# Kernel tuning notes

Measured on AMD Instinct MI355X. Metric: run time of the kernel, lower is better.

The kernel has to match this reference:

```python
import jax, jax.numpy as jnp
import numpy as np

B, N, C, H = 2, 2048, 1024, 16
D = C // H
SCALE = D ** -0.5


def setup_inputs() -> dict:
    key = jax.random.key(0)
    ks = jax.random.split(key, 4)
    s = 0.02
    return {
        "x": jax.random.normal(ks[0], (B, N, C), dtype=jnp.float32),
        "f": jax.random.normal(ks[1], (B, N, C), dtype=jnp.float32),
        "W_qkv": jax.random.normal(ks[2], (C, 3 * C), dtype=jnp.float32) * s,
        "W_proj": jax.random.normal(ks[3], (C, C), dtype=jnp.float32) * s,
        "b_proj": jnp.zeros((C,), dtype=jnp.float32),
    }


def reference(x, f, W_qkv, W_proj, b_proj):
    b, n, c = x.shape
    h, d = H, c // H
    # qkv projection -> (B,N,3,H,D) -> q,k,v each (B,H,N,D)
    qkv = (x @ W_qkv).reshape(b, n, 3, h, d)
    q = jnp.transpose(qkv[:, :, 0], (0, 2, 1, 3))
    k = jnp.transpose(qkv[:, :, 1], (0, 2, 1, 3))
    v = jnp.transpose(qkv[:, :, 2], (0, 2, 1, 3))
    # full NxN scores, faithful to the original manual MHA
    attn = jax.nn.softmax(jnp.einsum("bhqd,bhkd->bhqk", q, k) * SCALE, axis=-1)
    av = jnp.einsum("bhqk,bhkd->bhqd", attn, v)  # (B,H,N,D)
    # pre-residual output branch
    attn2gcn = jnp.transpose(av, (0, 2, 1, 3)).reshape(b, n, c)
    # residual fuse with f (reshaped per-head in torch; equivalent to flat add)
    fused = attn2gcn + f
    out = fused @ W_proj + b_proj
    return (out, attn2gcn)
```

## Files before the change

### kernel.cpp

```cpp
#include <hip/hip_runtime.h>
#include <hip/hip_bf16.h>

#define OUT1_OFF 4194304
#define QSCALE 0.1803368801111204f

typedef __attribute__((ext_vector_type(8))) short bf16x8;
typedef __attribute__((ext_vector_type(4))) float f32x4;

__device__ __forceinline__ unsigned short f2bf(float x) {
    unsigned u = __float_as_uint(x);
    u += 0x7FFFu + ((u >> 16) & 1u);
    return (unsigned short)(u >> 16);
}

__device__ __forceinline__ void gl2lds16(const unsigned short* g, unsigned short* l) {
    __builtin_amdgcn_global_load_lds(
        (const __attribute__((address_space(1))) unsigned int*)g,
        (__attribute__((address_space(3))) unsigned int*)l, 16, 0, 0);
}

__global__ __launch_bounds__(256) void prep(const float* __restrict__ x,
                                            const float* __restrict__ Wqkv,
                                            const float* __restrict__ Wproj,
                                            unsigned short* __restrict__ xb,
                                            unsigned short* __restrict__ wqkvT,
                                            unsigned short* __restrict__ wprojT) {
    __shared__ float T[64][65];
    const int bid = blockIdx.x, tid = threadIdx.x;
    if (bid < 4096) {
        int i = bid * 256 + tid;
        float4 v = reinterpret_cast<const float4*>(x)[i];
        ushort4 o = make_ushort4(f2bf(v.x), f2bf(v.y), f2bf(v.z), f2bf(v.w));
        reinterpret_cast<ushort4*>(xb)[i] = o;
        return;
    }
    const float* in; unsigned short* out; int Nd, bx, by;
    if (bid < 4864) { int t = bid - 4096; in = Wqkv;  out = wqkvT;  Nd = 3072; bx = t % 48; by = t / 48; }
    else            { int t = bid - 4864; in = Wproj; out = wprojT; Nd = 1024; bx = t % 16; by = t / 16; }
    const int Kd = 1024;
    const int r0 = by * 64, c0 = bx * 64;
    const int tr = tid >> 3, tc = (tid & 7) * 8;
#pragma unroll
    for (int rr = 0; rr < 64; rr += 32) {
        const float4* p = reinterpret_cast<const float4*>(&in[(r0 + tr + rr) * Nd + c0 + tc]);
        float4 v0 = p[0], v1 = p[1];
        T[tr + rr][tc + 0] = v0.x; T[tr + rr][tc + 1] = v0.y;
        T[tr + rr][tc + 2] = v0.z; T[tr + rr][tc + 3] = v0.w;
        T[tr + rr][tc + 4] = v1.x; T[tr + rr][tc + 5] = v1.y;
        T[tr + rr][tc + 6] = v1.z; T[tr + rr][tc + 7] = v1.w;
    }
    __syncthreads();
#pragma unroll
    for (int rr = 0; rr < 64; rr += 32) {
        int orow = tr + rr;
        ushort4 o0 = make_ushort4(f2bf(T[tc + 0][orow]), f2bf(T[tc + 1][orow]),
                                  f2bf(T[tc + 2][orow]), f2bf(T[tc + 3][orow]));
        ushort4 o1 = make_ushort4(f2bf(T[tc + 4][orow]), f2bf(T[tc + 5][orow]),
                                  f2bf(T[tc + 6][orow]), f2bf(T[tc + 7][orow]));
        unsigned short* dst = &out[(c0 + orow) * Kd + r0 + tc];
        *reinterpret_cast<ushort4*>(dst) = o0;
        *reinterpret_cast<ushort4*>(dst + 4) = o1;
    }
}

__global__ __launch_bounds__(256) void gemm_qkv(const unsigned short* __restrict__ A,
                                                const unsigned short* __restrict__ Bt,
                                                unsigned short* __restrict__ qb,
                                                unsigned short* __restrict__ kb,
                                                unsigned short* __restrict__ vtb) {
    __shared__ __align__(16) unsigned short Sh[32768];
    const int tid = threadIdx.x;
    const int w = tid >> 6, lane = tid & 63, quad = lane >> 4, l15 = lane & 15;
    const int m0 = blockIdx.y * 128, n0 = blockIdx.x * 128;
    const int wm = (w & 1) * 64, wn = (w >> 1) * 64;
    const int nbase = n0 + wn;
    const int t = nbase >> 10;
    const bool qk = (t < 2);
    const int sw = (l15 & 7) << 3;
    f32x4 acc[4][4] = {};

#define QKV_STAGE(K0, BUF) do {                                               \
        unsigned short* As_ = &Sh[(BUF) * 16384];                             \
        unsigned short* Bs_ = As_ + 8192;                                     \
        _Pragma("unroll")                                                     \
        for (int tt = 0; tt < 4; ++tt) {                                      \
            int c = tt * 256 + tid;                                           \
            int row = c >> 3, jg = ((c & 7) ^ (row & 7)) * 8;                 \
            gl2lds16(&A[(m0 + row) * 1024 + (K0) + jg], &As_[c * 8]);         \
            gl2lds16(&Bt[(n0 + row) * 1024 + (K0) + jg], &Bs_[c * 8]);        \
        } } while (0)

    auto compute = [&](int buf) {
        const unsigned short* As_ = &Sh[buf * 16384];
        const unsigned short* Bs_ = As_ + 8192;
#pragma unroll
        for (int kk = 0; kk < 2; ++kk) {
            bf16x8 af[4], bfr[4];
#pragma unroll
            for (int i = 0; i < 4; ++i)
                af[i] = *reinterpret_cast<const bf16x8*>(
                    &As_[(wm + i * 16 + l15) * 64 + ((((kk * 4 + quad) << 3) ^ sw))]);
#pragma unroll
            for (int j = 0; j < 4; ++j)
                bfr[j] = *reinterpret_cast<const bf16x8*>(
                    &Bs_[(wn + j * 16 + l15) * 64 + ((((kk * 4 + quad) << 3) ^ sw))]);
            if (qk) {
#pragma unroll
                for (int i = 0; i < 4; ++i)
#pragma unroll
                    for (int j = 0; j < 4; ++j)
                        acc[i][j] = __builtin_amdgcn_mfma_f32_16x16x32_bf16(bfr[j], af[i], acc[i][j], 0, 0, 0);
            } else {
#pragma unroll
                for (int i = 0; i < 4; ++i)
#pragma unroll
                    for (int j = 0; j < 4; ++j)
                        acc[i][j] = __builtin_amdgcn_mfma_f32_16x16x32_bf16(af[i], bfr[j], acc[i][j], 0, 0, 0);
            }
        }
    };

    QKV_STAGE(0, 0);
    for (int k0 = 0; k0 < 1024; k0 += 128) {
        __syncthreads();
        QKV_STAGE(k0 + 64, 1);
        compute(0);
        __syncthreads();
        if (k0 + 128 < 1024) QKV_STAGE(k0 + 128, 0);
        compute(1);
    }
#undef QKV_STAGE
    __syncthreads();
    unsigned short* scr = Sh + w * 4608;
    const int mb = m0 + wm;
    const int b = mb >> 11;
    const int h = (nbase & 1023) >> 6;
    const float sc = (t == 0) ? QSCALE : 1.f;
    if (qk) {
#pragma unroll
        for (int i = 0; i < 4; ++i) {
            int row = i * 16 + l15;
#pragma unroll
            for (int j = 0; j < 4; ++j) {
                unsigned short h0 = f2bf(acc[i][j][0] * sc), h1 = f2bf(acc[i][j][1] * sc);
                unsigned short h2 = f2bf(acc[i][j][2] * sc), h3 = f2bf(acc[i][j][3] * sc);
                uint2 pk = make_uint2((unsigned)h0 | ((unsigned)h1 << 16),
                                      (unsigned)h2 | ((unsigned)h3 << 16));
                *reinterpret_cast<uint2*>(&scr[row * 72 + j * 16 + quad * 4]) = pk;
            }
        }
        asm volatile("s_waitcnt lgkmcnt(0)" ::: "memory");
        unsigned short* dst = (t == 0 ? qb : kb) + (((b * 16 + h) * 2048) + (mb & 2047)) * 64;
#pragma unroll
        for (int p = 0; p < 8; ++p) {
            int idx = p * 64 + lane;
            *reinterpret_cast<uint4*>(&dst[idx * 8]) =
                *reinterpret_cast<const uint4*>(&scr[(idx >> 3) * 72 + (idx & 7) * 8]);
        }
    } else {
        const int kblk = (mb & 2047) >> 6;
#pragma unroll
        for (int i = 0; i < 4; ++i) {
            int slot0 = ((i & 2) << 4) | (quad << 3) | ((i & 1) << 2);
#pragma unroll
            for (int j = 0; j < 4; ++j) {
                unsigned short h0 = f2bf(acc[i][j][0]), h1 = f2bf(acc[i][j][1]);
                unsigned short h2 = f2bf(acc[i][j][2]), h3 = f2bf(acc[i][j][3]);
                uint2 pk = make_uint2((unsigned)h0 | ((unsigned)h1 << 16),
                                      (unsigned)h2 | ((unsigned)h3 << 16));
                *reinterpret_cast<uint2*>(&scr[(j * 16 + l15) * 72 + slot0]) = pk;
            }
        }
        asm volatile("s_waitcnt lgkmcnt(0)" ::: "memory");
        unsigned short* vtile = vtb + (((b * 16 + h) * 32) + kblk) * 4096;
#pragma unroll
        for (int p = 0; p < 8; ++p) {
            int idx = p * 64 + lane;
            *reinterpret_cast<uint4*>(&vtile[idx * 8]) =
                *reinterpret_cast<const uint4*>(&scr[(idx >> 3) * 72 + (idx & 7) * 8]);
        }
    }
}

__global__ __launch_bounds__(512, 4) void attn_kernel(const unsigned short* __restrict__ qb,
                                                      const unsigned short* __restrict__ kb,
                                                      const unsigned short* __restrict__ vtb,
                                                      const float* __restrict__ f,
                                                      float* __restrict__ attn2_out,
                                                      unsigned short* __restrict__ fusedb) {
    __shared__ __align__(16) unsigned char SMEM[69632];
    unsigned short* S16 = reinterpret_cast<unsigned short*>(SMEM);
    const int tid = threadIdx.x;
    const int w = tid >> 6, lane = tid & 63, quad = lane >> 4, l15 = lane & 15;
    const int qg = w & 3, kh = w >> 2;
    const int bh = blockIdx.x;
    const int q0w = blockIdx.y * 128 + qg * 32;
    const unsigned short* qr = &qb[(bh * 2048 + q0w + l15) * 64 + quad * 8];
    bf16x8 ql0 = *reinterpret_cast<const bf16x8*>(qr);
    bf16x8 ql1 = *reinterpret_cast<const bf16x8*>(qr + 32);
    bf16x8 ql2 = *reinterpret_cast<const bf16x8*>(qr + 1024);
    bf16x8 ql3 = *reinterpret_cast<const bf16x8*>(qr + 1056);
    const unsigned short* kt0 = kb + bh * 131072;
    const unsigned short* vt0 = vtb + bh * 131072;
    const int gu = (((tid & ~7) | ((tid & 7) ^ ((tid >> 3) & 7))) << 3);
    const int sw = (l15 & 7) << 3;
    f32x4 O0[4] = {}, O1[4] = {};
    f32x4 asum0 = {}, asum1 = {};
    bf16x8 ones;
#pragma unroll
    for (int j = 0; j < 8; ++j) ones[j] = (short)0x3F80;

#define STAGE(IT, BUF) do { unsigned short* db_ = &S16[(BUF) * 16384 + tid * 8]; \
        const int go_ = (IT) * 4096 + gu;                                        \
        gl2lds16(kt0 + go_, db_);                                                \
        gl2lds16(vt0 + go_, db_ + 4096);                                         \
        gl2lds16(kt0 + 65536 + go_, db_ + 8192);                                 \
        gl2lds16(vt0 + 65536 + go_, db_ + 12288); } while (0)

    auto body = [&](int buf) {
        const unsigned short* Kb = &S16[buf * 16384 + kh * 8192];
        const unsigned short* Vb = Kb + 4096;
        f32x4 Ta[4], Tb[4];
        __builtin_amdgcn_s_setprio(1);
#pragma unroll
        for (int s = 0; s < 4; ++s) {
            const unsigned short* kr = &Kb[(s * 16 + l15) * 64];
            bf16x8 k0 = *reinterpret_cast<const bf16x8*>(&kr[(quad << 3) ^ sw]);
            bf16x8 k1 = *reinterpret_cast<const bf16x8*>(&kr[((quad + 4) << 3) ^ sw]);
            f32x4 za = {}, zb = {};
            za = __builtin_amdgcn_mfma_f32_16x16x32_bf16(k0, ql0, za, 0, 0, 0);
            za = __builtin_amdgcn_mfma_f32_16x16x32_bf16(k1, ql1, za, 0, 0, 0);
            zb = __builtin_amdgcn_mfma_f32_16x16x32_bf16(k0, ql2, zb, 0, 0, 0);
            zb = __builtin_amdgcn_mfma_f32_16x16x32_bf16(k1, ql3, zb, 0, 0, 0);
            Ta[s] = za; Tb[s] = zb;
        }
        __builtin_amdgcn_s_setprio(0);
        float pa_[4][4], pb_[4][4];
#pragma unroll
        for (int s = 0; s < 4; ++s)
#pragma unroll
            for (int r = 0; r < 4; ++r) {
                pa_[s][r] = __builtin_amdgcn_exp2f(Ta[s][r]);
                pb_[s][r] = __builtin_amdgcn_exp2f(Tb[s][r]);
            }
        uint4 u0, u1, v0u, v1u;
        u0.x = __builtin_amdgcn_perm(__float_as_uint(pa_[0][1]), __float_as_uint(pa_[0][0]), 0x07060302u);
        u0.y = __builtin_amdgcn_perm(__float_as_uint(pa_[0][3]), __float_as_uint(pa_[0][2]), 0x07060302u);
        u0.z = __builtin_amdgcn_perm(__float_as_uint(pa_[1][1]), __float_as_uint(pa_[1][0]), 0x07060302u);
        u0.w = __builtin_amdgcn_perm(__float_as_uint(pa_[1][3]), __float_as_uint(pa_[1][2]), 0x07060302u);
        u1.x = __builtin_amdgcn_perm(__float_as_uint(pa_[2][1]), __float_as_uint(pa_[2][0]), 0x07060302u);
        u1.y = __builtin_amdgcn_perm(__float_as_uint(pa_[2][3]), __float_as_uint(pa_[2][2]), 0x07060302u);
        u1.z = __builtin_amdgcn_perm(__float_as_uint(pa_[3][1]), __float_as_uint(pa_[3][0]), 0x07060302u);
        u1.w = __builtin_amdgcn_perm(__float_as_uint(pa_[3][3]), __float_as_uint(pa_[3][2]), 0x07060302u);
        v0u.x = __builtin_amdgcn_perm(__float_as_uint(pb_[0][1]), __float_as_uint(pb_[0][0]), 0x07060302u);
        v0u.y = __builtin_amdgcn_perm(__float_as_uint(pb_[0][3]), __float_as_uint(pb_[0][2]), 0x07060302u);
        v0u.z = __builtin_amdgcn_perm(__float_as_uint(pb_[1][1]), __float_as_uint(pb_[1][0]), 0x07060302u);
        v0u.w = __builtin_amdgcn_perm(__float_as_uint(pb_[1][3]), __float_as_uint(pb_[1][2]), 0x07060302u);
        v1u.x = __builtin_amdgcn_perm(__float_as_uint(pb_[2][1]), __float_as_uint(pb_[2][0]), 0x07060302u);
        v1u.y = __builtin_amdgcn_perm(__float_as_uint(pb_[2][3]), __float_as_uint(pb_[2][2]), 0x07060302u);
        v1u.z = __builtin_amdgcn_perm(__float_as_uint(pb_[3][1]), __float_as_uint(pb_[3][0]), 0x07060302u);
        v1u.w = __builtin_amdgcn_perm(__float_as_uint(pb_[3][3]), __float_as_uint(pb_[3][2]), 0x07060302u);
        bf16x8 paa0 = __builtin_bit_cast(bf16x8, u0);
        bf16x8 paa1 = __builtin_bit_cast(bf16x8, u1);
        bf16x8 pba0 = __builtin_bit_cast(bf16x8, v0u);
        bf16x8 pba1 = __builtin_bit_cast(bf16x8, v1u);
        asum0 = __builtin_amdgcn_mfma_f32_16x16x32_bf16(paa0, ones, asum0, 0, 0, 0);
        asum0 = __builtin_amdgcn_mfma_f32_16x16x32_bf16(paa1, ones, asum0, 0, 0, 0);
        asum1 = __builtin_amdgcn_mfma_f32_16x16x32_bf16(pba0, ones, asum1, 0, 0, 0);
        asum1 = __builtin_amdgcn_mfma_f32_16x16x32_bf16(pba1, ones, asum1, 0, 0, 0);
        __builtin_amdgcn_s_setprio(1);
#pragma unroll
        for (int c4 = 0; c4 < 4; ++c4) {
            const unsigned short* vr = &Vb[(c4 * 16 + l15) * 64];
            bf16x8 v0 = *reinterpret_cast<const bf16x8*>(&vr[(quad << 3) ^ sw]);
            bf16x8 v1 = *reinterpret_cast<const bf16x8*>(&vr[((quad + 4) << 3) ^ sw]);
            O0[c4] = __builtin_amdgcn_mfma_f32_16x16x32_bf16(paa0, v0, O0[c4], 0, 0, 0);
            O0[c4] = __builtin_amdgcn_mfma_f32_16x16x32_bf16(paa1, v1, O0[c4], 0, 0, 0);
            O1[c4] = __builtin_amdgcn_mfma_f32_16x16x32_bf16(pba0, v0, O1[c4], 0, 0, 0);
            O1[c4] = __builtin_amdgcn_mfma_f32_16x16x32_bf16(pba1, v1, O1[c4], 0, 0, 0);
        }
        __builtin_amdgcn_s_setprio(0);
    };

    STAGE(0, 0);
    for (int it = 0; it < 16; it += 2) {
        __syncthreads();
        STAGE(it + 1, 1);
        body(0);
        __syncthreads();
        if (it + 2 < 16) STAGE(it + 2, 0);
        body(1);
    }
#undef STAGE

    __syncthreads();
    float* scr = reinterpret_cast<float*>(SMEM);
    {
        float* myr = scr + w * 2176;
#pragma unroll
        for (int c4 = 0; c4 < 4; ++c4) {
            int dcol = c4 * 16 + l15;
#pragma unroll
            for (int r = 0; r < 4; ++r) {
                myr[(quad * 4 + r) * 68 + dcol] = O0[c4][r];
                myr[(16 + quad * 4 + r) * 68 + dcol] = O1[c4][r];
            }
        }
        if (l15 == 0) {
#pragma unroll
            for (int r = 0; r < 4; ++r) {
                myr[(quad * 4 + r) * 68 + 64] = asum0[r];
                myr[(16 + quad * 4 + r) * 68 + 64] = asum1[r];
            }
        }
    }
    __syncthreads();
    const int b = bh >> 4, h = bh & 15;
    const float* rA = scr + qg * 2176;
    const float* rB = rA + 4 * 2176;
    const int row = kh * 16 + (lane >> 2);
    const int dq = (lane & 3) * 16;
    const int base = (b * 2048 + (q0w + row)) * 1024 + h * 64;
    const float den = rA[row * 68 + 64] + rB[row * 68 + 64];
    const float inv = 1.f / den;
#pragma unroll
    for (int j = 0; j < 4; ++j) {
        int d = dq + j * 4;
        f32x4 pa = *reinterpret_cast<const f32x4*>(&rA[row * 68 + d]);
        f32x4 pb = *reinterpret_cast<const f32x4*>(&rB[row * 68 + d]);
        float4 fv = *reinterpret_cast<const float4*>(&f[base + d]);
        float o0 = (pa[0] + pb[0]) * inv;
        float o1 = (pa[1] + pb[1]) * inv;
        float o2 = (pa[2] + pb[2]) * inv;
        float o3 = (pa[3] + pb[3]) * inv;
        *reinterpret_cast<float4*>(&attn2_out[base + d]) = make_float4(o0, o1, o2, o3);
        ushort4 pk = make_ushort4(f2bf(o0 + fv.x), f2bf(o1 + fv.y),
                                  f2bf(o2 + fv.z), f2bf(o3 + fv.w));
        *reinterpret_cast<ushort4*>(&fusedb[base + d]) = pk;
    }
}

__global__ __launch_bounds__(256) void gemm_proj(const unsigned short* __restrict__ A,
                                                 const unsigned short* __restrict__ Bt,
                                                 const float* __restrict__ bias,
                                                 float* __restrict__ out) {
    __shared__ __align__(16) unsigned short Sh[24576];
    const int tid = threadIdx.x;
    const int w = tid >> 6, lane = tid & 63, quad = lane >> 4, l15 = lane & 15;
    const int m0 = blockIdx.y * 128, n0 = blockIdx.x * 64;
    const int wm = (w & 1) * 64, wn = (w >> 1) * 32;
    const int sw = (l15 & 7) << 3;
    f32x4 acc[4][2] = {};

#define PROJ_STAGE(K0, BUF) do {                                              \
        unsigned short* As_ = &Sh[(BUF) * 12288];                             \
        unsigned short* Bs_ = As_ + 8192;                                     \
        _Pragma("unroll")                                                     \
        for (int tt = 0; tt < 4; ++tt) {                                      \
            int c = tt * 256 + tid;                                           \
            int row = c >> 3, jg = ((c & 7) ^ (row & 7)) * 8;                 \
            gl2lds16(&A[(m0 + row) * 1024 + (K0) + jg], &As_[c * 8]);         \
            if (tt < 2) gl2lds16(&Bt[(n0 + row) * 1024 + (K0) + jg], &Bs_[c * 8]); \
        } } while (0)

    auto compute = [&](int buf) {
        const unsigned short* As_ = &Sh[buf * 12288];
        const unsigned short* Bs_ = As_ + 8192;
#pragma unroll
        for (int kk = 0; kk < 2; ++kk) {
            bf16x8 af[4], bfr[2];
#pragma unroll
            for (int i = 0; i < 4; ++i)
                af[i] = *reinterpret_cast<const bf16x8*>(
                    &As_[(wm + i * 16 + l15) * 64 + ((((kk * 4 + quad) << 3) ^ sw))]);
#pragma unroll
            for (int j = 0; j < 2; ++j)
                bfr[j] = *reinterpret_cast<const bf16x8*>(
                    &Bs_[(wn + j * 16 + l15) * 64 + ((((kk * 4 + quad) << 3) ^ sw))]);
#pragma unroll
            for (int i = 0; i < 4; ++i)
#pragma unroll
                for (int j = 0; j < 2; ++j)
                    acc[i][j] = __builtin_amdgcn_mfma_f32_16x16x32_bf16(af[i], bfr[j], acc[i][j], 0, 0, 0);
        }
    };

    PROJ_STAGE(0, 0);
    for (int k0 = 0; k0 < 1024; k0 += 128) {
        __syncthreads();
        PROJ_STAGE(k0 + 64, 1);
        compute(0);
        __syncthreads();
        if (k0 + 128 < 1024) PROJ_STAGE(k0 + 128, 0);
        compute(1);
    }
#undef PROJ_STAGE

#pragma unroll
    for (int j = 0; j < 2; ++j) {
        int n = n0 + wn + j * 16 + l15;
        float bv = bias[n];
#pragma unroll
        for (int i = 0; i < 4; ++i)
#pragma unroll
            for (int r = 0; r < 4; ++r) {
                int m = m0 + wm + i * 16 + quad * 4 + r;
                out[m * 1024 + n] = acc[i][j][r] + bv;
            }
    }
}

extern "C" void kernel_launch(void* const* d_in, const int* in_sizes, int n_in,
                              void* d_out, int out_size, void* d_ws, size_t ws_size,
                              hipStream_t stream) {
    const float* x      = (const float*)d_in[0];
    const float* f      = (const float*)d_in[1];
    const float* W_qkv  = (const float*)d_in[2];
    const float* W_proj = (const float*)d_in[3];
    const float* b_proj = (const float*)d_in[4];
    float* out   = (float*)d_out;
    float* attn2 = out + OUT1_OFF;

    char* ws = (char*)d_ws;
    unsigned short* xb     = (unsigned short*)(ws);
    unsigned short* wqkvT  = (unsigned short*)(ws + 8388608);
    unsigned short* wprojT = (unsigned short*)(ws + 14680064);
    unsigned short* qb     = (unsigned short*)(ws + 16777216);
    unsigned short* kb     = (unsigned short*)(ws + 25165824);
    unsigned short* vtb    = (unsigned short*)(ws + 33554432);
    unsigned short* fusedb = (unsigned short*)(ws + 41943040);

    prep<<<5120, 256, 0, stream>>>(x, W_qkv, W_proj, xb, wqkvT, wprojT);
    gemm_qkv<<<dim3(24, 32), 256, 0, stream>>>(xb, wqkvT, qb, kb, vtb);
    attn_kernel<<<dim3(32, 16), 512, 0, stream>>>(qb, kb, vtb, f, attn2, fusedb);
    gemm_proj<<<dim3(16, 32), 256, 0, stream>>>(fusedb, wprojT, b_proj, out);
}
```

Measured before the change: 176.2 us.

## Software-pipeline attention loop: overlap QK^T of tile i with PV of tile i-1

```diff
diff --git a/kernel.cpp b/kernel.cpp
--- a/kernel.cpp
+++ b/kernel.cpp
@@ -209,17 +209,43 @@
     bf16x8 ones;
 #pragma unroll
     for (int j = 0; j < 8; ++j) ones[j] = (short)0x3F80;
-
-#define STAGE(IT, BUF) do { unsigned short* db_ = &S16[(BUF) * 16384 + tid * 8]; \
+    bf16x8 pA0 = {}, pA1 = {}, pA2 = {}, pA3 = {};
+    bf16x8 pB0 = {}, pB1 = {}, pB2 = {}, pB3 = {};
+
+#define BARX() do { __builtin_amdgcn_sched_barrier(0); __builtin_amdgcn_s_barrier(); \
+                    __builtin_amdgcn_sched_barrier(0); } while (0)
+#define VMW(N) asm volatile("s_waitcnt vmcnt(" #N ")" ::: "memory")
+#define STAGE_K(IT, B) do { unsigned short* kd_ = &S16[(B) * 8192 + tid * 8];    \
         const int go_ = (IT) * 4096 + gu;                                        \
-        gl2lds16(kt0 + go_, db_);                                                \
-        gl2lds16(vt0 + go_, db_ + 4096);                                         \
-        gl2lds16(kt0 + 65536 + go_, db_ + 8192);                                 \
-        gl2lds16(vt0 + 65536 + go_, db_ + 12288); } while (0)
-
-    auto body = [&](int buf) {
-        const unsigned short* Kb = &S16[buf * 16384 + kh * 8192];
-        const unsigned short* Vb = Kb + 4096;
+        gl2lds16(kt0 + go_, kd_);                                                \
+        gl2lds16(kt0 + 65536 + go_, kd_ + 4096); } while (0)
+#define STAGE_V(IT, B) do { unsigned short* vd_ = &S16[16384 + (B) * 8192 + tid * 8]; \
+        const int go_ = (IT) * 4096 + gu;                                        \
+        gl2lds16(vt0 + go_, vd_);                                                \
+        gl2lds16(vt0 + 65536 + go_, vd_ + 4096); } while (0)
+
+    auto pv = [&](int vbb, bf16x8& i0, bf16x8& i1, bf16x8& i2, bf16x8& i3) {
+        const unsigned short* Vb = &S16[16384 + vbb * 8192 + kh * 4096];
+        asum0 = __builtin_amdgcn_mfma_f32_16x16x32_bf16(i0, ones, asum0, 0, 0, 0);
+        asum0 = __builtin_amdgcn_mfma_f32_16x16x32_bf16(i1, ones, asum0, 0, 0, 0);
+        asum1 = __builtin_amdgcn_mfma_f32_16x16x32_bf16(i2, ones, asum1, 0, 0, 0);
+        asum1 = __builtin_amdgcn_mfma_f32_16x16x32_bf16(i3, ones, asum1, 0, 0, 0);
+#pragma unroll
+        for (int c4 = 0; c4 < 4; ++c4) {
+            const unsigned short* vr = &Vb[(c4 * 16 + l15) * 64];
+            bf16x8 v0 = *reinterpret_cast<const bf16x8*>(&vr[(quad << 3) ^ sw]);
+            bf16x8 v1 = *reinterpret_cast<const bf16x8*>(&vr[((quad + 4) << 3) ^ sw]);
+            O0[c4] = __builtin_amdgcn_mfma_f32_16x16x32_bf16(i0, v0, O0[c4], 0, 0, 0);
+            O0[c4] = __builtin_amdgcn_mfma_f32_16x16x32_bf16(i1, v1, O0[c4], 0, 0, 0);
+            O1[c4] = __builtin_amdgcn_mfma_f32_16x16x32_bf16(i2, v0, O1[c4], 0, 0, 0);
+            O1[c4] = __builtin_amdgcn_mfma_f32_16x16x32_bf16(i3, v1, O1[c4], 0, 0, 0);
+        }
+    };
+
+    auto step = [&](int kbb, int vbb,
+                    bf16x8& i0, bf16x8& i1, bf16x8& i2, bf16x8& i3,
+                    bf16x8& o0, bf16x8& o1, bf16x8& o2, bf16x8& o3, bool doPV) {
+        const unsigned short* Kb = &S16[kbb * 8192 + kh * 4096];
         f32x4 Ta[4], Tb[4];
         __builtin_amdgcn_s_setprio(1);
 #pragma unroll
@@ -234,6 +260,7 @@
             zb = __builtin_amdgcn_mfma_f32_16x16x32_bf16(k1, ql3, zb, 0, 0, 0);
             Ta[s] = za; Tb[s] = zb;
         }
+        if (doPV) pv(vbb, i0, i1, i2, i3);
         __builtin_amdgcn_s_setprio(0);
         float pa_[4][4], pb_[4][4];
 #pragma unroll
@@ -260,38 +287,35 @@
         v1u.y = __builtin_amdgcn_perm(__float_as_uint(pb_[2][3]), __float_as_uint(pb_[2][2]), 0x07060302u);
         v1u.z = __builtin_amdgcn_perm(__float_as_uint(pb_[3][1]), __float_as_uint(pb_[3][0]), 0x07060302u);
         v1u.w = __builtin_amdgcn_perm(__float_as_uint(pb_[3][3]), __float_as_uint(pb_[3][2]), 0x07060302u);
-        bf16x8 paa0 = __builtin_bit_cast(bf16x8, u0);
-        bf16x8 paa1 = __builtin_bit_cast(bf16x8, u1);
-        bf16x8 pba0 = __builtin_bit_cast(bf16x8, v0u);
-        bf16x8 pba1 = __builtin_bit_cast(bf16x8, v1u);
-        asum0 = __builtin_amdgcn_mfma_f32_16x16x32_bf16(paa0, ones, asum0, 0, 0, 0);
-        asum0 = __builtin_amdgcn_mfma_f32_16x16x32_bf16(paa1, ones, asum0, 0, 0, 0);
-        asum1 = __builtin_amdgcn_mfma_f32_16x16x32_bf16(pba0, ones, asum1, 0, 0, 0);
-        asum1 = __builtin_amdgcn_mfma_f32_16x16x32_bf16(pba1, ones, asum1, 0, 0, 0);
-        __builtin_amdgcn_s_setprio(1);
-#pragma unroll
-        for (int c4 = 0; c4 < 4; ++c4) {
-            const unsigned short* vr = &Vb[(c4 * 16 + l15) * 64];
-            bf16x8 v0 = *reinterpret_cast<const bf16x8*>(&vr[(quad << 3) ^ sw]);
-            bf16x8 v1 = *reinterpret_cast<const bf16x8*>(&vr[((quad + 4) << 3) ^ sw]);
-            O0[c4] = __builtin_amdgcn_mfma_f32_16x16x32_bf16(paa0, v0, O0[c4], 0, 0, 0);
-            O0[c4] = __builtin_amdgcn_mfma_f32_16x16x32_bf16(paa1, v1, O0[c4], 0, 0, 0);
-            O1[c4] = __builtin_amdgcn_mfma_f32_16x16x32_bf16(pba0, v0, O1[c4], 0, 0, 0);
-            O1[c4] = __builtin_amdgcn_mfma_f32_16x16x32_bf16(pba1, v1, O1[c4], 0, 0, 0);
-        }
-        __builtin_amdgcn_s_setprio(0);
+        o0 = __builtin_bit_cast(bf16x8, u0);
+        o1 = __builtin_bit_cast(bf16x8, u1);
+        o2 = __builtin_bit_cast(bf16x8, v0u);
+        o3 = __builtin_bit_cast(bf16x8, v1u);
     };
 
-    STAGE(0, 0);
-    for (int it = 0; it < 16; it += 2) {
-        __syncthreads();
-        STAGE(it + 1, 1);
-        body(0);
-        __syncthreads();
-        if (it + 2 < 16) STAGE(it + 2, 0);
-        body(1);
-    }
-#undef STAGE
+    STAGE_K(0, 0); STAGE_V(0, 0); STAGE_K(1, 1);
+    VMW(2); BARX();
+    step(0, 0, pA0, pA1, pA2, pA3, pA0, pA1, pA2, pA3, false);
+    BARX(); STAGE_K(2, 0); STAGE_V(1, 1); VMW(4); BARX();
+    for (int i = 1; i < 13; i += 2) {
+        step(1, 0, pA0, pA1, pA2, pA3, pB0, pB1, pB2, pB3, true);
+        BARX(); STAGE_K(i + 2, 1); STAGE_V(i + 1, 0); VMW(4); BARX();
+        step(0, 1, pB0, pB1, pB2, pB3, pA0, pA1, pA2, pA3, true);
+        BARX(); STAGE_K(i + 3, 0); STAGE_V(i + 2, 1); VMW(4); BARX();
+    }
+    step(1, 0, pA0, pA1, pA2, pA3, pB0, pB1, pB2, pB3, true);
+    BARX(); STAGE_K(15, 1); STAGE_V(14, 0); VMW(4); BARX();
+    step(0, 1, pB0, pB1, pB2, pB3, pA0, pA1, pA2, pA3, true);
+    BARX(); STAGE_V(15, 1); VMW(2); BARX();
+    step(1, 0, pA0, pA1, pA2, pA3, pB0, pB1, pB2, pB3, true);
+    VMW(0); BARX();
+    __builtin_amdgcn_s_setprio(1);
+    pv(1, pB0, pB1, pB2, pB3);
+    __builtin_amdgcn_s_setprio(0);
+#undef STAGE_K
+#undef STAGE_V
+#undef BARX
+#undef VMW
 
     __syncthreads();
     float* scr = reinterpret_cast<float*>(SMEM);
```

Result: slower. 198.1 us (+12.4%).

## Restage QKV GEMM A-tile through registers to cut LDS and raise occupancy

Applied to the files above, without the earlier changes.

```diff
diff --git a/kernel.cpp b/kernel.cpp
--- a/kernel.cpp
+++ b/kernel.cpp
@@ -27,16 +27,20 @@
                                             unsigned short* __restrict__ wprojT) {
     __shared__ float T[64][65];
     const int bid = blockIdx.x, tid = threadIdx.x;
-    if (bid < 4096) {
-        int i = bid * 256 + tid;
-        float4 v = reinterpret_cast<const float4*>(x)[i];
-        ushort4 o = make_ushort4(f2bf(v.x), f2bf(v.y), f2bf(v.z), f2bf(v.w));
-        reinterpret_cast<ushort4*>(xb)[i] = o;
+    if (bid < 1024) {
+        int base = bid * 1024 + tid;
+#pragma unroll
+        for (int j = 0; j < 4; ++j) {
+            int i = base + j * 256;
+            float4 v = reinterpret_cast<const float4*>(x)[i];
+            ushort4 o = make_ushort4(f2bf(v.x), f2bf(v.y), f2bf(v.z), f2bf(v.w));
+            reinterpret_cast<ushort4*>(xb)[i] = o;
+        }
         return;
     }
     const float* in; unsigned short* out; int Nd, bx, by;
-    if (bid < 4864) { int t = bid - 4096; in = Wqkv;  out = wqkvT;  Nd = 3072; bx = t % 48; by = t / 48; }
-    else            { int t = bid - 4864; in = Wproj; out = wprojT; Nd = 1024; bx = t % 16; by = t / 16; }
+    if (bid < 1792) { int t = bid - 1024; in = Wqkv;  out = wqkvT;  Nd = 3072; bx = t % 48; by = t / 48; }
+    else            { int t = bid - 1792; in = Wproj; out = wprojT; Nd = 1024; bx = t % 16; by = t / 16; }
     const int Kd = 1024;
     const int r0 = by * 64, c0 = bx * 64;
     const int tr = tid >> 3, tc = (tid & 7) * 8;
@@ -63,12 +67,12 @@
     }
 }
 
-__global__ __launch_bounds__(256) void gemm_qkv(const unsigned short* __restrict__ A,
-                                                const unsigned short* __restrict__ Bt,
-                                                unsigned short* __restrict__ qb,
-                                                unsigned short* __restrict__ kb,
-                                                unsigned short* __restrict__ vtb) {
-    __shared__ __align__(16) unsigned short Sh[32768];
+__global__ __launch_bounds__(256, 3) void gemm_qkv(const unsigned short* __restrict__ A,
+                                                   const unsigned short* __restrict__ Bt,
+                                                   unsigned short* __restrict__ qb,
+                                                   unsigned short* __restrict__ kb,
+                                                   unsigned short* __restrict__ vtb) {
+    __shared__ __align__(16) unsigned short Sh[24576];
     const int tid = threadIdx.x;
     const int w = tid >> 6, lane = tid & 63, quad = lane >> 4, l15 = lane & 15;
     const int m0 = blockIdx.y * 128, n0 = blockIdx.x * 128;
@@ -78,21 +82,31 @@
     const bool qk = (t < 2);
     const int sw = (l15 & 7) << 3;
     f32x4 acc[4][4] = {};
-
-#define QKV_STAGE(K0, BUF) do {                                               \
-        unsigned short* As_ = &Sh[(BUF) * 16384];                             \
-        unsigned short* Bs_ = As_ + 8192;                                     \
-        _Pragma("unroll")                                                     \
-        for (int tt = 0; tt < 4; ++tt) {                                      \
-            int c = tt * 256 + tid;                                           \
-            int row = c >> 3, jg = ((c & 7) ^ (row & 7)) * 8;                 \
-            gl2lds16(&A[(m0 + row) * 1024 + (K0) + jg], &As_[c * 8]);         \
-            gl2lds16(&Bt[(n0 + row) * 1024 + (K0) + jg], &Bs_[c * 8]);        \
-        } } while (0)
+    int aoff[4], boff[4], loff[4];
+#pragma unroll
+    for (int tt = 0; tt < 4; ++tt) {
+        int c = tt * 256 + tid;
+        int row = c >> 3, jg = ((c & 7) ^ (row & 7)) * 8;
+        aoff[tt] = (m0 + row) * 1024 + jg;
+        boff[tt] = (n0 + row) * 1024 + jg;
+        loff[tt] = c * 8;
+    }
+    uint4 areg[4];
+
+#define VMW(N) asm volatile("s_waitcnt vmcnt(" #N ")" ::: "memory")
+#define LGK0() asm volatile("s_waitcnt lgkmcnt(0)" ::: "memory")
+#define BARX() do { __builtin_amdgcn_sched_barrier(0); __builtin_amdgcn_s_barrier(); \
+                    __builtin_amdgcn_sched_barrier(0); } while (0)
+#define LOAD_A(K0) do { _Pragma("unroll") for (int tt = 0; tt < 4; ++tt)          \
+        areg[tt] = *reinterpret_cast<const uint4*>(&A[aoff[tt] + (K0)]); } while (0)
+#define WRITE_A() do { _Pragma("unroll") for (int tt = 0; tt < 4; ++tt)           \
+        *reinterpret_cast<uint4*>(&Sh[loff[tt]]) = areg[tt]; } while (0)
+#define STAGE_B(K0, BUF) do { _Pragma("unroll") for (int tt = 0; tt < 4; ++tt)    \
+        gl2lds16(&Bt[boff[tt] + (K0)], &Sh[8192 + (BUF) * 8192 + loff[tt]]); } while (0)
 
     auto compute = [&](int buf) {
-        const unsigned short* As_ = &Sh[buf * 16384];
-        const unsigned short* Bs_ = As_ + 8192;
+        const unsigned short* As_ = Sh;
+        const unsigned short* Bs_ = &Sh[8192 + buf * 8192];
 #pragma unroll
         for (int kk = 0; kk < 2; ++kk) {
             bf16x8 af[4], bfr[4];
@@ -120,16 +134,30 @@
         }
     };
 
-    QKV_STAGE(0, 0);
-    for (int k0 = 0; k0 < 1024; k0 += 128) {
-        __syncthreads();
-        QKV_STAGE(k0 + 64, 1);
-        compute(0);
-        __syncthreads();
-        if (k0 + 128 < 1024) QKV_STAGE(k0 + 128, 0);
-        compute(1);
-    }
-#undef QKV_STAGE
+    LOAD_A(0); STAGE_B(0, 0);
+    VMW(4);
+    WRITE_A();
+    LOAD_A(64); STAGE_B(64, 1);
+    LGK0();
+    VMW(8);
+    BARX();
+    for (int k = 0; k < 16; ++k) {
+        compute(k & 1);
+        BARX();
+        if (k == 15) break;
+        VMW(4);
+        WRITE_A();
+        if (k + 2 < 16) { LOAD_A((k + 2) * 64); STAGE_B((k + 2) * 64, k & 1); }
+        LGK0();
+        if (k + 2 < 16) VMW(8); else VMW(0);
+        BARX();
+    }
+#undef LOAD_A
+#undef WRITE_A
+#undef STAGE_B
+#undef VMW
+#undef LGK0
+#undef BARX
     __syncthreads();
     unsigned short* scr = Sh + w * 4608;
     const int mb = m0 + wm;
@@ -430,7 +458,7 @@
     unsigned short* vtb    = (unsigned short*)(ws + 33554432);
     unsigned short* fusedb = (unsigned short*)(ws + 41943040);
 
-    prep<<<5120, 256, 0, stream>>>(x, W_qkv, W_proj, xb, wqkvT, wprojT);
+    prep<<<2048, 256, 0, stream>>>(x, W_qkv, W_proj, xb, wqkvT, wprojT);
     gemm_qkv<<<dim3(24, 32), 256, 0, stream>>>(xb, wqkvT, qb, kb, vtb);
     attn_kernel<<<dim3(32, 16), 512, 0, stream>>>(qb, kb, vtb, f, attn2, fusedb);
     gemm_proj<<<dim3(16, 32), 256, 0, stream>>>(fusedb, wprojT, b_proj, out);
```

After: 254.3 us. +44.3%, slower.
